# Performance work log

Hardware: AMD Instinct MI355X
Metric: run time of the kernel (lower is better)

The kernel has to match this reference:

```python
import jax, jax.numpy as jnp
import numpy as np

INV_SCALE = 22.627416997969522  # sqrt(512), divisor as in qk.div(inv_scale_factor)
DROPOUT_P = 0.1
DROPOUT_KEY = 42  # fixed key so the reference is deterministic


def setup_inputs() -> dict:
    key = jax.random.key(0)
    k1, k2, k3 = jax.random.split(key, 3)
    return {
        "in1": jax.random.normal(k1, (4, 4096, 512), dtype=jnp.float32),   # [B, S, d]
        "in2": jax.random.normal(k2, (512, 512), dtype=jnp.float32),       # [K, d]
        "value": jax.random.normal(k3, (512, 4096), dtype=jnp.float32),    # [K, dv] (self.value param)
    }


def reference(in1, in2, value):
    # qk = in1 @ in2^T : [B, S, K]
    qk = jnp.einsum('bsd,kd->bsk', in1, in2)
    scaled_qk = qk / INV_SCALE
    probs = jax.nn.softmax(scaled_qk, axis=-1)
    # dropout with fixed key (training-mode semantics, inverted scaling)
    keep = jax.random.bernoulli(jax.random.key(DROPOUT_KEY), 1.0 - DROPOUT_P, probs.shape)
    dropped = jnp.where(keep, probs / (1.0 - DROPOUT_P), 0.0)
    # output = dropped @ value : [B, S, dv]
    return jnp.einsum('bsk,kv->bsv', dropped, value)
```

## Files before the change

### kernel.cpp

```cpp
#include <hip/hip_runtime.h>
#include <stdint.h>


typedef __bf16 bf16x8 __attribute__((ext_vector_type(8)));
typedef unsigned short u16x8 __attribute__((ext_vector_type(8)));
typedef float f32x4 __attribute__((ext_vector_type(4)));

#define SM_SCALE 4.419417382415922e-02f
#define DROP_SCALE (1.0f / 0.9f)

__device__ __forceinline__ unsigned short f2bf(float f) {
  uint32_t u = __float_as_uint(f);
  uint32_t r = (u + 0x7FFFu + ((u >> 16) & 1u)) >> 16;
  return (unsigned short)r;
}
__device__ __forceinline__ float bf2f(unsigned short h) {
  return __uint_as_float(((uint32_t)h) << 16);
}

__device__ __forceinline__ void async16(const void* g, void* l) {
  __builtin_amdgcn_global_load_lds(
      (__attribute__((address_space(1))) uint32_t*)g,
      (__attribute__((address_space(3))) uint32_t*)l, 16, 0, 0);
}

__device__ __forceinline__ void threefry2x32(uint32_t x0, uint32_t x1,
                                             uint32_t& o0, uint32_t& o1) {
  const uint32_t K0 = 0u, K1 = 42u;
  const uint32_t K2 = K0 ^ K1 ^ 0x1BD11BDAu;
  x0 += K0; x1 += K1;
#define TF_R(rot) { x0 += x1; x1 = (x1 << rot) | (x1 >> (32 - rot)); x1 ^= x0; }
  TF_R(13) TF_R(15) TF_R(26) TF_R(6)  x0 += K1; x1 += K2 + 1u;
  TF_R(17) TF_R(29) TF_R(16) TF_R(24) x0 += K2; x1 += K0 + 2u;
  TF_R(13) TF_R(15) TF_R(26) TF_R(6)  x0 += K0; x1 += K1 + 3u;
  TF_R(17) TF_R(29) TF_R(16) TF_R(24) x0 += K1; x1 += K2 + 4u;
  TF_R(13) TF_R(15) TF_R(26) TF_R(6)  x0 += K2; x1 += K0 + 5u;
#undef TF_R
  o0 = x0; o1 = x1;
}

__device__ __forceinline__ bool drop_keep(uint32_t idx) {
  uint32_t o0, o1;
  threefry2x32(0u, idx, o0, o1);
  uint32_t bits = o0 ^ o1;
  float u = __uint_as_float((bits >> 9) | 0x3f800000u) - 1.0f;
  return u < 0.9f;
}

__global__ __launch_bounds__(256) void k_vt(const float* __restrict__ v,
                                            unsigned short* __restrict__ vt) {
  __shared__ float tile[32][33];
  const int nb = blockIdx.x;
  const int kb = blockIdx.y;
  const int tx = threadIdx.x & 31, ty = threadIdx.x >> 5;
#pragma unroll
  for (int yy = 0; yy < 4; ++yy) {
    int row = ty + yy * 8;
    tile[row][tx] = v[(size_t)(kb * 32 + row) * 4096 + nb * 32 + tx];
  }
  __syncthreads();
#pragma unroll
  for (int yy = 0; yy < 4; ++yy) {
    int row = ty + yy * 8;
    vt[(size_t)(nb * 32 + row) * 512 + kb * 32 + tx] = f2bf(tile[tx][row]);
  }
}

__global__ __launch_bounds__(256) void k_split(const float* __restrict__ src,
                                               unsigned short* __restrict__ hi,
                                               unsigned short* __restrict__ lo,
                                               int n4) {
  int i = blockIdx.x * 256 + threadIdx.x;
  if (i >= n4) return;
  float4 v = reinterpret_cast<const float4*>(src)[i];
  ushort4 h, l;
  h.x = f2bf(v.x); l.x = f2bf(v.x - bf2f(h.x));
  h.y = f2bf(v.y); l.y = f2bf(v.y - bf2f(h.y));
  h.z = f2bf(v.z); l.z = f2bf(v.z - bf2f(h.z));
  h.w = f2bf(v.w); l.w = f2bf(v.w - bf2f(h.w));
  reinterpret_cast<ushort4*>(hi)[i] = h;
  reinterpret_cast<ushort4*>(lo)[i] = l;
}

__global__ __launch_bounds__(512) void k_qk(const float* __restrict__ in1,
                                            const unsigned short* __restrict__ B2hi,
                                            const unsigned short* __restrict__ B2lo,
                                            unsigned short* __restrict__ P) {
  __shared__ unsigned short lB[512][72];
  __shared__ float redm[4][32], reds[4][32];

  const int tid = threadIdx.x;
  const int l = tid & 63, w = tid >> 6;
  const int wr = w >> 2, wc = w & 3;
  const int g = l >> 4, c16 = l & 15;
  const int brow = blockIdx.x * 32;

  f32x4 acc[8] = {};

  for (int kt = 0; kt < 16; ++kt) {
    const int k0 = kt * 32;
#pragma unroll
    for (int i = 0; i < 8; ++i) {
      int c = i * 512 + tid;
      int col = c >> 3, half = (c >> 2) & 1, sub = c & 3;
      const unsigned short* src = (half ? B2lo : B2hi) + (size_t)col * 512 + k0 + sub * 8;
      *reinterpret_cast<u16x8*>(&lB[col][half * 32 + sub * 8]) =
          *reinterpret_cast<const u16x8*>(src);
    }
    const int arow = brow + wr * 16 + c16;
    float4 v0 = *reinterpret_cast<const float4*>(in1 + (size_t)arow * 512 + k0 + g * 8);
    float4 v1 = *reinterpret_cast<const float4*>(in1 + (size_t)arow * 512 + k0 + g * 8 + 4);
    bf16x8 ahi, alo;
    {
      float vv[8] = {v0.x, v0.y, v0.z, v0.w, v1.x, v1.y, v1.z, v1.w};
      unsigned short h[8], lo8[8];
#pragma unroll
      for (int e = 0; e < 8; ++e) {
        h[e] = f2bf(vv[e]);
        lo8[e] = f2bf(vv[e] - bf2f(h[e]));
      }
      ahi = *reinterpret_cast<const bf16x8*>(h);
      alo = *reinterpret_cast<const bf16x8*>(lo8);
    }
    __syncthreads();
#pragma unroll
    for (int j = 0; j < 8; ++j) {
      const int col = wc * 128 + j * 16 + c16;
      bf16x8 bh = *reinterpret_cast<const bf16x8*>(&lB[col][g * 8]);
      bf16x8 bl = *reinterpret_cast<const bf16x8*>(&lB[col][32 + g * 8]);
      acc[j] = __builtin_amdgcn_mfma_f32_16x16x32_bf16(ahi, bh, acc[j], 0, 0, 0);
      acc[j] = __builtin_amdgcn_mfma_f32_16x16x32_bf16(alo, bh, acc[j], 0, 0, 0);
      acc[j] = __builtin_amdgcn_mfma_f32_16x16x32_bf16(ahi, bl, acc[j], 0, 0, 0);
    }
    __syncthreads();
  }

  const int rowbase = wr * 16 + g * 4;
  float mx[4] = {-3.4e38f, -3.4e38f, -3.4e38f, -3.4e38f};
#pragma unroll
  for (int j = 0; j < 8; ++j)
#pragma unroll
    for (int r = 0; r < 4; ++r) {
      acc[j][r] *= SM_SCALE;
      mx[r] = fmaxf(mx[r], acc[j][r]);
    }
#pragma unroll
  for (int s = 1; s < 16; s <<= 1)
#pragma unroll
    for (int r = 0; r < 4; ++r) mx[r] = fmaxf(mx[r], __shfl_xor(mx[r], s, 64));
  if (c16 == 0) {
#pragma unroll
    for (int r = 0; r < 4; ++r) redm[wc][rowbase + r] = mx[r];
  }
  __syncthreads();
  float rmax[4], sum[4] = {0.f, 0.f, 0.f, 0.f};
#pragma unroll
  for (int r = 0; r < 4; ++r)
    rmax[r] = fmaxf(fmaxf(redm[0][rowbase + r], redm[1][rowbase + r]),
                    fmaxf(redm[2][rowbase + r], redm[3][rowbase + r]));
#pragma unroll
  for (int j = 0; j < 8; ++j)
#pragma unroll
    for (int r = 0; r < 4; ++r) {
      float e = expf(acc[j][r] - rmax[r]);
      acc[j][r] = e;
      sum[r] += e;
    }
#pragma unroll
  for (int s = 1; s < 16; s <<= 1)
#pragma unroll
    for (int r = 0; r < 4; ++r) sum[r] += __shfl_xor(sum[r], s, 64);
  if (c16 == 0) {
#pragma unroll
    for (int r = 0; r < 4; ++r) reds[wc][rowbase + r] = sum[r];
  }
  __syncthreads();
  float scl[4];
#pragma unroll
  for (int r = 0; r < 4; ++r)
    scl[r] = DROP_SCALE / (reds[0][rowbase + r] + reds[1][rowbase + r] +
                           reds[2][rowbase + r] + reds[3][rowbase + r]);

#pragma unroll
  for (int j = 0; j < 8; ++j) {
    const int col = wc * 128 + j * 16 + c16;
#pragma unroll
    for (int r = 0; r < 4; ++r) {
      uint32_t idx = (uint32_t)(brow + rowbase + r) * 512u + (uint32_t)col;
      float pv = drop_keep(idx) ? acc[j][r] * scl[r] : 0.0f;
      P[idx] = f2bf(pv);
    }
  }
}

__global__ __launch_bounds__(512) void k_pv(const unsigned short* __restrict__ P,
                                            const unsigned short* __restrict__ VT,
                                            float* __restrict__ out) {
  __shared__ unsigned short lds[65536];
  const int tid = threadIdx.x;
  const int l = tid & 63, w = tid >> 6;
  const int wr = w >> 2, wc = w & 3;
  const int g = l >> 4, c16 = l & 15;

  const int bid = blockIdx.x;
  const int x = (bid & 7) * 128 + (bid >> 3);
  const int brow = (x >> 4) * 256;
  const int bcol = (x & 15) * 256;

  const int lr_base = w * 16 + (l >> 2);
  const int p = l & 3;

  f32x4 acc[8][4] = {};

#define STAGE(t, kh, b)                                                        \
  {                                                                            \
    const int kofs = (t) * 64 + (kh) * 32;                                     \
    _Pragma("unroll")                                                          \
    for (int i = 0; i < 2; ++i) {                                              \
      int lr = i * 128 + lr_base;                                              \
      int gs = p ^ ((lr >> 1) & 3);                                            \
      unsigned short* dA = lds + ((b) * 2 + (kh)) * 8192 + (i * 512 + w * 64) * 8; \
      async16(P + (size_t)(brow + lr) * 512 + kofs + gs * 8, dA);              \
      async16(VT + (size_t)(bcol + lr) * 512 + kofs + gs * 8, dA + 32768);     \
    }                                                                          \
  }

#define FRAGS(b, kh)                                                           \
  const unsigned short* rbase = lds + ((b) * 2 + (kh)) * 8192;                 \
  bf16x8 a[8], bb[4];                                                          \
  _Pragma("unroll")                                                            \
  for (int mi = 0; mi < 8; ++mi) {                                             \
    int ar = wr * 128 + mi * 16 + c16;                                         \
    a[mi] = *reinterpret_cast<const bf16x8*>(rbase + ar * 32 +                 \
                                             (g ^ ((ar >> 1) & 3)) * 8);       \
  }                                                                            \
  _Pragma("unroll")                                                            \
  for (int nj = 0; nj < 4; ++nj) {                                             \
    int br = wc * 64 + nj * 16 + c16;                                          \
    bb[nj] = *reinterpret_cast<const bf16x8*>(rbase + 32768 + br * 32 +        \
                                              (g ^ ((br >> 1) & 3)) * 8);      \
  }

#define MFMA32()                                                               \
  __builtin_amdgcn_s_setprio(1);                                               \
  _Pragma("unroll")                                                            \
  for (int mi = 0; mi < 8; ++mi)                                               \
    _Pragma("unroll")                                                          \
    for (int nj = 0; nj < 4; ++nj)                                             \
      acc[mi][nj] = __builtin_amdgcn_mfma_f32_16x16x32_bf16(a[mi], bb[nj],     \
                                                            acc[mi][nj], 0, 0, 0); \
  __builtin_amdgcn_s_setprio(0);

  STAGE(0, 0, 0) STAGE(0, 1, 0) STAGE(1, 0, 1)

  for (int t = 0; t < 7; ++t) {
    const int cur = t & 1, nxt = cur ^ 1;
    asm volatile("s_waitcnt vmcnt(8)" ::: "memory");
    __builtin_amdgcn_s_barrier();
    STAGE(t + 1, 1, nxt)
    {
      FRAGS(cur, 0)
      MFMA32()
    }
    asm volatile("s_waitcnt vmcnt(8)" ::: "memory");
    __builtin_amdgcn_s_barrier();
    if (t < 6) STAGE(t + 2, 0, cur)
    {
      FRAGS(cur, 1)
      MFMA32()
    }
  }
  asm volatile("s_waitcnt vmcnt(4)" ::: "memory");
  __builtin_amdgcn_s_barrier();
  {
    FRAGS(1, 0)
    MFMA32()
  }
  asm volatile("s_waitcnt vmcnt(0)" ::: "memory");
  __builtin_amdgcn_s_barrier();
  {
    FRAGS(1, 1)
    MFMA32()
  }
#undef STAGE
#undef FRAGS
#undef MFMA32

#pragma unroll
  for (int i = 0; i < 8; ++i)
#pragma unroll
    for (int r = 0; r < 4; ++r) {
      const size_t row = (size_t)(brow + wr * 128 + i * 16 + g * 4 + r);
      float* o = out + row * 4096 + bcol + wc * 64 + c16;
#pragma unroll
      for (int j = 0; j < 4; ++j) o[j * 16] = acc[i][j][r];
    }
}

extern "C" void kernel_launch(void* const* d_in, const int* in_sizes, int n_in,
                              void* d_out, int out_size, void* d_ws, size_t ws_size,
                              hipStream_t stream) {
  (void)in_sizes; (void)n_in; (void)out_size; (void)ws_size;
  const float* in1   = (const float*)d_in[0];
  const float* in2   = (const float*)d_in[1];
  const float* value = (const float*)d_in[2];
  float* out = (float*)d_out;

  unsigned short* vT    = (unsigned short*)d_ws;
  unsigned short* Pb    = vT + 2097152;
  unsigned short* in2hi = Pb + 8388608;
  unsigned short* in2lo = in2hi + 262144;

  k_vt<<<dim3(128, 16), dim3(256), 0, stream>>>(value, vT);
  k_split<<<dim3(256), dim3(256), 0, stream>>>(in2, in2hi, in2lo, 65536);
  k_qk<<<dim3(512), dim3(512), 0, stream>>>(in1, in2hi, in2lo, Pb);
  k_pv<<<dim3(1024), dim3(512), 0, stream>>>(Pb, vT, out);
}
```

Measured before the change: 186.5 us.

## Drop in2 low-part split in QK and enlarge row tile to 64

Replaces the three-term split-bf16 QK product with two terms by casting in2 to a single bf16 copy, so the B-lo LDS loads and one MFMA per tile disappear. The QK kernel now handles 64 rows per block with 2 column-wave groups of 256 columns each, which halves the grid, halves the B tile staged per row block, and shrinks the softmax reductions. This costs accuracy in the QK logits and raises register pressure from 16 accumulators per wave, with a launch bound of 4.

```diff
diff --git a/kernel.cpp b/kernel.cpp
--- a/kernel.cpp
+++ b/kernel.cpp
@@ -66,46 +66,39 @@
   }
 }
 
-__global__ __launch_bounds__(256) void k_split(const float* __restrict__ src,
-                                               unsigned short* __restrict__ hi,
-                                               unsigned short* __restrict__ lo,
-                                               int n4) {
+__global__ __launch_bounds__(256) void k_cast(const float* __restrict__ src,
+                                              unsigned short* __restrict__ dst,
+                                              int n4) {
   int i = blockIdx.x * 256 + threadIdx.x;
   if (i >= n4) return;
   float4 v = reinterpret_cast<const float4*>(src)[i];
-  ushort4 h, l;
-  h.x = f2bf(v.x); l.x = f2bf(v.x - bf2f(h.x));
-  h.y = f2bf(v.y); l.y = f2bf(v.y - bf2f(h.y));
-  h.z = f2bf(v.z); l.z = f2bf(v.z - bf2f(h.z));
-  h.w = f2bf(v.w); l.w = f2bf(v.w - bf2f(h.w));
-  reinterpret_cast<ushort4*>(hi)[i] = h;
-  reinterpret_cast<ushort4*>(lo)[i] = l;
-}
-
-__global__ __launch_bounds__(512) void k_qk(const float* __restrict__ in1,
-                                            const unsigned short* __restrict__ B2hi,
-                                            const unsigned short* __restrict__ B2lo,
-                                            unsigned short* __restrict__ P) {
-  __shared__ unsigned short lB[512][72];
-  __shared__ float redm[4][32], reds[4][32];
+  ushort4 h;
+  h.x = f2bf(v.x); h.y = f2bf(v.y); h.z = f2bf(v.z); h.w = f2bf(v.w);
+  reinterpret_cast<ushort4*>(dst)[i] = h;
+}
+
+__global__ __launch_bounds__(512, 4) void k_qk(const float* __restrict__ in1,
+                                               const unsigned short* __restrict__ B2,
+                                               unsigned short* __restrict__ P) {
+  __shared__ unsigned short lB[512][36];
+  __shared__ float redm[2][64], reds[2][64];
 
   const int tid = threadIdx.x;
   const int l = tid & 63, w = tid >> 6;
-  const int wr = w >> 2, wc = w & 3;
+  const int wr = w >> 1, wc = w & 1;
   const int g = l >> 4, c16 = l & 15;
-  const int brow = blockIdx.x * 32;
-
-  f32x4 acc[8] = {};
+  const int brow = blockIdx.x * 64;
+
+  f32x4 acc[16] = {};
 
   for (int kt = 0; kt < 16; ++kt) {
     const int k0 = kt * 32;
 #pragma unroll
-    for (int i = 0; i < 8; ++i) {
+    for (int i = 0; i < 4; ++i) {
       int c = i * 512 + tid;
-      int col = c >> 3, half = (c >> 2) & 1, sub = c & 3;
-      const unsigned short* src = (half ? B2lo : B2hi) + (size_t)col * 512 + k0 + sub * 8;
-      *reinterpret_cast<u16x8*>(&lB[col][half * 32 + sub * 8]) =
-          *reinterpret_cast<const u16x8*>(src);
+      int col = c >> 2, sub = c & 3;
+      *reinterpret_cast<u16x8*>(&lB[col][sub * 8]) =
+          *reinterpret_cast<const u16x8*>(B2 + (size_t)col * 512 + k0 + sub * 8);
     }
     const int arow = brow + wr * 16 + c16;
     float4 v0 = *reinterpret_cast<const float4*>(in1 + (size_t)arow * 512 + k0 + g * 8);
@@ -124,13 +117,11 @@
     }
     __syncthreads();
 #pragma unroll
-    for (int j = 0; j < 8; ++j) {
-      const int col = wc * 128 + j * 16 + c16;
+    for (int j = 0; j < 16; ++j) {
+      const int col = wc * 256 + j * 16 + c16;
       bf16x8 bh = *reinterpret_cast<const bf16x8*>(&lB[col][g * 8]);
-      bf16x8 bl = *reinterpret_cast<const bf16x8*>(&lB[col][32 + g * 8]);
       acc[j] = __builtin_amdgcn_mfma_f32_16x16x32_bf16(ahi, bh, acc[j], 0, 0, 0);
       acc[j] = __builtin_amdgcn_mfma_f32_16x16x32_bf16(alo, bh, acc[j], 0, 0, 0);
-      acc[j] = __builtin_amdgcn_mfma_f32_16x16x32_bf16(ahi, bl, acc[j], 0, 0, 0);
     }
     __syncthreads();
   }
@@ -138,7 +129,7 @@
   const int rowbase = wr * 16 + g * 4;
   float mx[4] = {-3.4e38f, -3.4e38f, -3.4e38f, -3.4e38f};
 #pragma unroll
-  for (int j = 0; j < 8; ++j)
+  for (int j = 0; j < 16; ++j)
 #pragma unroll
     for (int r = 0; r < 4; ++r) {
       acc[j][r] *= SM_SCALE;
@@ -156,10 +147,9 @@
   float rmax[4], sum[4] = {0.f, 0.f, 0.f, 0.f};
 #pragma unroll
   for (int r = 0; r < 4; ++r)
-    rmax[r] = fmaxf(fmaxf(redm[0][rowbase + r], redm[1][rowbase + r]),
-                    fmaxf(redm[2][rowbase + r], redm[3][rowbase + r]));
-#pragma unroll
-  for (int j = 0; j < 8; ++j)
+    rmax[r] = fmaxf(redm[0][rowbase + r], redm[1][rowbase + r]);
+#pragma unroll
+  for (int j = 0; j < 16; ++j)
 #pragma unroll
     for (int r = 0; r < 4; ++r) {
       float e = expf(acc[j][r] - rmax[r]);
@@ -178,12 +168,11 @@
   float scl[4];
 #pragma unroll
   for (int r = 0; r < 4; ++r)
-    scl[r] = DROP_SCALE / (reds[0][rowbase + r] + reds[1][rowbase + r] +
-                           reds[2][rowbase + r] + reds[3][rowbase + r]);
-
-#pragma unroll
-  for (int j = 0; j < 8; ++j) {
-    const int col = wc * 128 + j * 16 + c16;
+    scl[r] = DROP_SCALE / (reds[0][rowbase + r] + reds[1][rowbase + r]);
+
+#pragma unroll
+  for (int j = 0; j < 16; ++j) {
+    const int col = wc * 256 + j * 16 + c16;
 #pragma unroll
     for (int r = 0; r < 4; ++r) {
       uint32_t idx = (uint32_t)(brow + rowbase + r) * 512u + (uint32_t)col;
@@ -306,13 +295,12 @@
   const float* value = (const float*)d_in[2];
   float* out = (float*)d_out;
 
-  unsigned short* vT    = (unsigned short*)d_ws;
-  unsigned short* Pb    = vT + 2097152;
-  unsigned short* in2hi = Pb + 8388608;
-  unsigned short* in2lo = in2hi + 262144;
+  unsigned short* vT   = (unsigned short*)d_ws;
+  unsigned short* Pb   = vT + 2097152;
+  unsigned short* in2b = Pb + 8388608;
 
   k_vt<<<dim3(128, 16), dim3(256), 0, stream>>>(value, vT);
-  k_split<<<dim3(256), dim3(256), 0, stream>>>(in2, in2hi, in2lo, 65536);
-  k_qk<<<dim3(512), dim3(512), 0, stream>>>(in1, in2hi, in2lo, Pb);
+  k_cast<<<dim3(256), dim3(256), 0, stream>>>(in2, in2b, 65536);
+  k_qk<<<dim3(256), dim3(512), 0, stream>>>(in1, in2b, Pb);
   k_pv<<<dim3(1024), dim3(512), 0, stream>>>(Pb, vT, out);
 }
```

New measurement: 168.5 us. 9.7% less time.
